# Performance work log

Measured on AMD Instinct MI355X. Metric: run time of the kernel, lower is better.

## Reference

```python
import jax, jax.numpy as jnp
import numpy as np

FACTOR = 8
IN_DIM = 4096
OUT_DIM = 4096


def setup_inputs() -> dict:
    key = jax.random.key(0)
    kx, ka, ks = jax.random.split(key, 3)
    x = jax.random.normal(kx, (4, 2048, IN_DIM), dtype=jnp.float32)
    a = jax.random.normal(ka, (FACTOR, FACTOR, FACTOR), dtype=jnp.float32) * 0.1
    s = jax.random.normal(ks, (FACTOR, OUT_DIM // FACTOR, IN_DIM // FACTOR), dtype=jnp.float32) * 0.05
    return {"x": x, "a": a, "s": s}


def reference(x, a, s):
    f = a.shape[0]
    out_dim = a.shape[1] * s.shape[1]
    in_dim = a.shape[2] * s.shape[2]
    # Batched Kronecker product: (f, a_rows*k, a_cols*p) then sum over batch dim f.
    # weight[a*k + ?, c*p + ?] = sum_b a[b, ar, ac] * s[b, kr, pc]
    p = jnp.einsum('bac,bkp->bakcp', a, s)  # (f, f, out/f, f, in/f)
    weight = p.reshape(f, out_dim, in_dim).sum(axis=0)  # (out, in)
    return x @ weight.T
```

## Files before the change

### kernel.cpp

```cpp
#include <hip/hip_runtime.h>
#include <hip/hip_bf16.h>
#include <stdint.h>

namespace {

constexpr int MTOT = 8192;
constexpr int NTOT = 4096;
constexpr int KTOT = 4096;

constexpr int BM = 256, BN = 256, BK = 32;
constexpr int NT = KTOT / BK;

typedef __attribute__((ext_vector_type(8))) short bf16x8;
typedef __attribute__((ext_vector_type(4))) float f32x4;

__device__ inline unsigned short to_bf16(float f) {
    union { float f; uint32_t u; } v; v.f = f;
    return (unsigned short)((v.u + 0x7FFFu + ((v.u >> 16) & 1u)) >> 16);
}

__global__ __launch_bounds__(256) void convert_x_kernel(const float* __restrict__ x,
                                                        unsigned short* __restrict__ xb) {
    int idx = blockIdx.x * 256 + threadIdx.x;
    const f32x4* xv = reinterpret_cast<const f32x4*>(x);
    f32x4 v0 = xv[2 * idx];
    f32x4 v1 = xv[2 * idx + 1];
    union { bf16x8 v; unsigned short s[8]; } o;
    o.s[0] = to_bf16(v0.x); o.s[1] = to_bf16(v0.y);
    o.s[2] = to_bf16(v0.z); o.s[3] = to_bf16(v0.w);
    o.s[4] = to_bf16(v1.x); o.s[5] = to_bf16(v1.y);
    o.s[6] = to_bf16(v1.z); o.s[7] = to_bf16(v1.w);
    reinterpret_cast<bf16x8*>(xb)[idx] = o.v;
}

__global__ __launch_bounds__(256) void gen_w_kernel(const float* __restrict__ a,
                                                    const float* __restrict__ s,
                                                    unsigned short* __restrict__ w) {
    int idx = blockIdx.x * 256 + threadIdx.x;
    int o  = idx >> 9;
    int i8 = idx & 511;
    int i0 = i8 * 8;
    int obig = o >> 9, orow = o & 511;
    int ibig = i0 >> 9, icol = i0 & 511;

    float acc[8];
#pragma unroll
    for (int j = 0; j < 8; ++j) acc[j] = 0.f;

#pragma unroll
    for (int b = 0; b < 8; ++b) {
        float av = a[b * 64 + obig * 8 + ibig];
        const f32x4* sv = reinterpret_cast<const f32x4*>(s + b * 512 * 512 + orow * 512 + icol);
        f32x4 s0 = sv[0], s1 = sv[1];
        acc[0] += av * s0.x; acc[1] += av * s0.y; acc[2] += av * s0.z; acc[3] += av * s0.w;
        acc[4] += av * s1.x; acc[5] += av * s1.y; acc[6] += av * s1.z; acc[7] += av * s1.w;
    }
    union { bf16x8 v; unsigned short q[8]; } ov;
#pragma unroll
    for (int j = 0; j < 8; ++j) ov.q[j] = to_bf16(acc[j]);
    reinterpret_cast<bf16x8*>(w)[idx] = ov.v;
}

__global__ __launch_bounds__(512, 2)
void gemm_bt_kernel(const unsigned short* __restrict__ A,
                    const unsigned short* __restrict__ B,
                    float* __restrict__ C) {
    __shared__ __align__(16) unsigned short As[4][BM][BK];
    __shared__ __align__(16) unsigned short Bs[4][BN][BK];

    int bid = blockIdx.x;
    int swz = (bid & 7) * 64 + (bid >> 3);
    int bm = swz >> 4;
    int bn = swz & 15;

    int tid  = threadIdx.x;
    int wid  = tid >> 6;
    int lane = tid & 63;
    int wm = wid >> 2, wn = wid & 3;

    int srow  = lane >> 2;
    int sslot = (lane & 3) ^ ((srow >> 1) & 3);
    const unsigned short* ag0 = A + (size_t)(bm * BM + wid * 16 + srow) * KTOT + sslot * 8;
    const unsigned short* ag1 = ag0 + (size_t)128 * KTOT;
    const unsigned short* bg0 = B + (size_t)(bn * BN + wid * 16 + srow) * KTOT + sslot * 8;
    const unsigned short* bg1 = bg0 + (size_t)128 * KTOT;

    int rl    = lane & 15;
    int rslot = (lane >> 4) ^ ((rl >> 1) & 3);

    f32x4 acc[8][4];
#pragma unroll
    for (int m = 0; m < 8; ++m)
#pragma unroll
        for (int n = 0; n < 4; ++n) acc[m][n] = (f32x4)0.f;

    auto STAGE_A = [&](int s, int k0) {
        __builtin_amdgcn_global_load_lds(
            (const __attribute__((address_space(1))) void*)(ag0 + k0),
            (__attribute__((address_space(3))) void*)&As[s][wid * 16][0], 16, 0, 0);
        __builtin_amdgcn_global_load_lds(
            (const __attribute__((address_space(1))) void*)(ag1 + k0),
            (__attribute__((address_space(3))) void*)&As[s][128 + wid * 16][0], 16, 0, 0);
    };
    auto STAGE_B = [&](int s, int k0) {
        __builtin_amdgcn_global_load_lds(
            (const __attribute__((address_space(1))) void*)(bg0 + k0),
            (__attribute__((address_space(3))) void*)&Bs[s][wid * 16][0], 16, 0, 0);
        __builtin_amdgcn_global_load_lds(
            (const __attribute__((address_space(1))) void*)(bg1 + k0),
            (__attribute__((address_space(3))) void*)&Bs[s][128 + wid * 16][0], 16, 0, 0);
    };

    auto LDA = [&](int s, int mi) -> bf16x8 {
        return *reinterpret_cast<const bf16x8*>(&As[s][wm * 128 + mi * 16 + rl][rslot * 8]);
    };
    auto LDB = [&](int s, int ni) -> bf16x8 {
        return *reinterpret_cast<const bf16x8*>(&Bs[s][wn * 64 + ni * 16 + rl][rslot * 8]);
    };

    bf16x8 fa[4], fb[4], ga[4], pa[4], pb[4];

    STAGE_A(0, 0);          STAGE_B(0, 0);
    STAGE_A(1, BK);         STAGE_B(1, BK);
    STAGE_A(2, 2 * BK);     STAGE_B(2, 2 * BK);
    asm volatile("s_waitcnt vmcnt(4)" ::: "memory");
    __builtin_amdgcn_s_barrier();
#pragma unroll
    for (int m = 0; m < 4; ++m) fa[m] = LDA(0, m);
#pragma unroll
    for (int n = 0; n < 4; ++n) fb[n] = LDB(0, n);

    for (int tb = 0; tb < NT; tb += 4) {
#pragma unroll
        for (int u = 0; u < 4; ++u) {
            const int t  = tb + u;
            const int s  = u;
            const int nx = (u + 1) & 3;
            const int ss = (u + 3) & 3;
            const bool st = (t + 3) < NT;
            const int k0 = (t + 3) * BK;

#pragma unroll
            for (int m = 0; m < 4; ++m) ga[m] = LDA(s, m + 4);
            if (st) STAGE_A(ss, k0);
            asm volatile("s_waitcnt lgkmcnt(4)" ::: "memory");
            __builtin_amdgcn_sched_barrier(0);
            __builtin_amdgcn_s_setprio(1);
#pragma unroll
            for (int m = 0; m < 4; ++m)
#pragma unroll
                for (int n = 0; n < 4; ++n)
                    acc[m][n] = __builtin_amdgcn_mfma_f32_16x16x32_bf16(fa[m], fb[n], acc[m][n], 0, 0, 0);
            __builtin_amdgcn_s_setprio(0);

#pragma unroll
            for (int m = 0; m < 4; ++m) pa[m] = LDA(nx, m);
#pragma unroll
            for (int n = 0; n < 4; ++n) pb[n] = LDB(nx, n);
            if (st) STAGE_B(ss, k0);
            asm volatile("s_waitcnt lgkmcnt(8)" ::: "memory");
            __builtin_amdgcn_sched_barrier(0);
            __builtin_amdgcn_s_setprio(1);
#pragma unroll
            for (int m = 0; m < 4; ++m)
#pragma unroll
                for (int n = 0; n < 4; ++n)
                    acc[m + 4][n] = __builtin_amdgcn_mfma_f32_16x16x32_bf16(ga[m], fb[n], acc[m + 4][n], 0, 0, 0);
            __builtin_amdgcn_s_setprio(0);

            asm volatile("s_waitcnt vmcnt(4)" ::: "memory");
            __builtin_amdgcn_s_barrier();

#pragma unroll
            for (int m = 0; m < 4; ++m) fa[m] = pa[m];
#pragma unroll
            for (int n = 0; n < 4; ++n) fb[n] = pb[n];
        }
    }

    int crow0 = bm * BM + wm * 128 + (lane >> 4) * 4;
    int ccol0 = bn * BN + wn * 64 + (lane & 15);
#pragma unroll
    for (int m = 0; m < 8; ++m)
#pragma unroll
        for (int n = 0; n < 4; ++n)
#pragma unroll
            for (int j = 0; j < 4; ++j) {
                size_t r = (size_t)(crow0 + m * 16 + j);
                size_t c = (size_t)(ccol0 + n * 16);
                C[r * NTOT + c] = acc[m][n][j];
            }
}

}

extern "C" void kernel_launch(void* const* d_in, const int* in_sizes, int n_in,
                              void* d_out, int out_size, void* d_ws, size_t ws_size,
                              hipStream_t stream) {
    const float* x = (const float*)d_in[0];
    const float* a = (const float*)d_in[1];
    const float* s = (const float*)d_in[2];
    float* out = (float*)d_out;

    unsigned short* xb = (unsigned short*)d_ws;
    unsigned short* wb = xb + (size_t)MTOT * KTOT;

    convert_x_kernel<<<(MTOT * KTOT / 8) / 256, 256, 0, stream>>>(x, xb);
    gen_w_kernel<<<(NTOT * KTOT / 8) / 256, 256, 0, stream>>>(a, s, wb);
    gemm_bt_kernel<<<(MTOT / 256) * (NTOT / 256), 512, 0, stream>>>(xb, wb, out);
}
```

Before: 293.9 us.

## Use 4 waves per block with 128x128 warp tiles in bf16 GEMM

Shrinks the GEMM block from 8 waves to 4. Each wave now computes a 128x128 output tile with 64 accumulators instead of 128x64, and staging is rebalanced so each wave loads 4 row groups. The register prefetch of next-stage fragments across iterations is removed: each iteration loads all of its A/B fragments from LDS and then issues two MFMA halves. This cuts LDS read traffic per FLOP, but it raises register pressure, halves waves per CU, and removes the LDS-to-register overlap.

```diff
diff --git a/kernel.cpp b/kernel.cpp
--- a/kernel.cpp
+++ b/kernel.cpp
@@ -61,7 +61,7 @@
     reinterpret_cast<bf16x8*>(w)[idx] = ov.v;
 }
 
-__global__ __launch_bounds__(512, 2)
+__global__ __launch_bounds__(256, 1)
 void gemm_bt_kernel(const unsigned short* __restrict__ A,
                     const unsigned short* __restrict__ B,
                     float* __restrict__ C) {
@@ -76,114 +76,101 @@
     int tid  = threadIdx.x;
     int wid  = tid >> 6;
     int lane = tid & 63;
-    int wm = wid >> 2, wn = wid & 3;
+    int wm = wid >> 1, wn = wid & 1;
 
     int srow  = lane >> 2;
     int sslot = (lane & 3) ^ ((srow >> 1) & 3);
-    const unsigned short* ag0 = A + (size_t)(bm * BM + wid * 16 + srow) * KTOT + sslot * 8;
-    const unsigned short* ag1 = ag0 + (size_t)128 * KTOT;
-    const unsigned short* bg0 = B + (size_t)(bn * BN + wid * 16 + srow) * KTOT + sslot * 8;
-    const unsigned short* bg1 = bg0 + (size_t)128 * KTOT;
+    const unsigned short* ag = A + (size_t)(bm * BM + wid * 64 + srow) * KTOT + sslot * 8;
+    const unsigned short* bg = B + (size_t)(bn * BN + wid * 64 + srow) * KTOT + sslot * 8;
 
     int rl    = lane & 15;
     int rslot = (lane >> 4) ^ ((rl >> 1) & 3);
 
-    f32x4 acc[8][4];
+    f32x4 acc[8][8];
 #pragma unroll
     for (int m = 0; m < 8; ++m)
 #pragma unroll
-        for (int n = 0; n < 4; ++n) acc[m][n] = (f32x4)0.f;
+        for (int n = 0; n < 8; ++n) acc[m][n] = (f32x4)0.f;
 
     auto STAGE_A = [&](int s, int k0) {
-        __builtin_amdgcn_global_load_lds(
-            (const __attribute__((address_space(1))) void*)(ag0 + k0),
-            (__attribute__((address_space(3))) void*)&As[s][wid * 16][0], 16, 0, 0);
-        __builtin_amdgcn_global_load_lds(
-            (const __attribute__((address_space(1))) void*)(ag1 + k0),
-            (__attribute__((address_space(3))) void*)&As[s][128 + wid * 16][0], 16, 0, 0);
+#pragma unroll
+        for (int g = 0; g < 4; ++g)
+            __builtin_amdgcn_global_load_lds(
+                (const __attribute__((address_space(1))) void*)(ag + (size_t)g * 16 * KTOT + k0),
+                (__attribute__((address_space(3))) void*)&As[s][wid * 64 + g * 16][0], 16, 0, 0);
     };
     auto STAGE_B = [&](int s, int k0) {
-        __builtin_amdgcn_global_load_lds(
-            (const __attribute__((address_space(1))) void*)(bg0 + k0),
-            (__attribute__((address_space(3))) void*)&Bs[s][wid * 16][0], 16, 0, 0);
-        __builtin_amdgcn_global_load_lds(
-            (const __attribute__((address_space(1))) void*)(bg1 + k0),
-            (__attribute__((address_space(3))) void*)&Bs[s][128 + wid * 16][0], 16, 0, 0);
+#pragma unroll
+        for (int g = 0; g < 4; ++g)
+            __builtin_amdgcn_global_load_lds(
+                (const __attribute__((address_space(1))) void*)(bg + (size_t)g * 16 * KTOT + k0),
+                (__attribute__((address_space(3))) void*)&Bs[s][wid * 64 + g * 16][0], 16, 0, 0);
     };
 
     auto LDA = [&](int s, int mi) -> bf16x8 {
         return *reinterpret_cast<const bf16x8*>(&As[s][wm * 128 + mi * 16 + rl][rslot * 8]);
     };
     auto LDB = [&](int s, int ni) -> bf16x8 {
-        return *reinterpret_cast<const bf16x8*>(&Bs[s][wn * 64 + ni * 16 + rl][rslot * 8]);
+        return *reinterpret_cast<const bf16x8*>(&Bs[s][wn * 128 + ni * 16 + rl][rslot * 8]);
     };
-
-    bf16x8 fa[4], fb[4], ga[4], pa[4], pb[4];
 
     STAGE_A(0, 0);          STAGE_B(0, 0);
     STAGE_A(1, BK);         STAGE_B(1, BK);
     STAGE_A(2, 2 * BK);     STAGE_B(2, 2 * BK);
-    asm volatile("s_waitcnt vmcnt(4)" ::: "memory");
+    asm volatile("s_waitcnt vmcnt(16)" ::: "memory");
     __builtin_amdgcn_s_barrier();
-#pragma unroll
-    for (int m = 0; m < 4; ++m) fa[m] = LDA(0, m);
-#pragma unroll
-    for (int n = 0; n < 4; ++n) fb[n] = LDB(0, n);
 
     for (int tb = 0; tb < NT; tb += 4) {
 #pragma unroll
         for (int u = 0; u < 4; ++u) {
             const int t  = tb + u;
             const int s  = u;
-            const int nx = (u + 1) & 3;
             const int ss = (u + 3) & 3;
             const bool st = (t + 3) < NT;
             const int k0 = (t + 3) * BK;
 
+            bf16x8 fa[8], fb[8];
+            if (st) STAGE_A(ss, k0);
 #pragma unroll
-            for (int m = 0; m < 4; ++m) ga[m] = LDA(s, m + 4);
-            if (st) STAGE_A(ss, k0);
+            for (int m = 0; m < 8; ++m) fa[m] = LDA(s, m);
+#pragma unroll
+            for (int n = 0; n < 4; ++n) fb[n] = LDB(s, n);
+            if (st) STAGE_B(ss, k0);
+#pragma unroll
+            for (int n = 4; n < 8; ++n) fb[n] = LDB(s, n);
+
             asm volatile("s_waitcnt lgkmcnt(4)" ::: "memory");
             __builtin_amdgcn_sched_barrier(0);
             __builtin_amdgcn_s_setprio(1);
 #pragma unroll
-            for (int m = 0; m < 4; ++m)
+            for (int m = 0; m < 8; ++m)
 #pragma unroll
                 for (int n = 0; n < 4; ++n)
                     acc[m][n] = __builtin_amdgcn_mfma_f32_16x16x32_bf16(fa[m], fb[n], acc[m][n], 0, 0, 0);
             __builtin_amdgcn_s_setprio(0);
 
-#pragma unroll
-            for (int m = 0; m < 4; ++m) pa[m] = LDA(nx, m);
-#pragma unroll
-            for (int n = 0; n < 4; ++n) pb[n] = LDB(nx, n);
-            if (st) STAGE_B(ss, k0);
-            asm volatile("s_waitcnt lgkmcnt(8)" ::: "memory");
+            asm volatile("s_waitcnt lgkmcnt(0)" ::: "memory");
             __builtin_amdgcn_sched_barrier(0);
             __builtin_amdgcn_s_setprio(1);
 #pragma unroll
-            for (int m = 0; m < 4; ++m)
+            for (int m = 0; m < 8; ++m)
 #pragma unroll
-                for (int n = 0; n < 4; ++n)
-                    acc[m + 4][n] = __builtin_amdgcn_mfma_f32_16x16x32_bf16(ga[m], fb[n], acc[m + 4][n], 0, 0, 0);
+                for (int n = 4; n < 8; ++n)
+                    acc[m][n] = __builtin_amdgcn_mfma_f32_16x16x32_bf16(fa[m], fb[n], acc[m][n], 0, 0, 0);
             __builtin_amdgcn_s_setprio(0);
 
-            asm volatile("s_waitcnt vmcnt(4)" ::: "memory");
+            if (st) { asm volatile("s_waitcnt vmcnt(8)" ::: "memory"); }
+            else    { asm volatile("s_waitcnt vmcnt(0)" ::: "memory"); }
             __builtin_amdgcn_s_barrier();
-
-#pragma unroll
-            for (int m = 0; m < 4; ++m) fa[m] = pa[m];
-#pragma unroll
-            for (int n = 0; n < 4; ++n) fb[n] = pb[n];
         }
     }
 
     int crow0 = bm * BM + wm * 128 + (lane >> 4) * 4;
-    int ccol0 = bn * BN + wn * 64 + (lane & 15);
+    int ccol0 = bn * BN + wn * 128 + (lane & 15);
 #pragma unroll
     for (int m = 0; m < 8; ++m)
 #pragma unroll
-        for (int n = 0; n < 4; ++n)
+        for (int n = 0; n < 8; ++n)
 #pragma unroll
             for (int j = 0; j < 4; ++j) {
                 size_t r = (size_t)(crow0 + m * 16 + j);
@@ -207,5 +194,5 @@
 
     convert_x_kernel<<<(MTOT * KTOT / 8) / 256, 256, 0, stream>>>(x, xb);
     gen_w_kernel<<<(NTOT * KTOT / 8) / 256, 256, 0, stream>>>(a, s, wb);
-    gemm_bt_kernel<<<(MTOT / 256) * (NTOT / 256), 512, 0, stream>>>(xb, wb, out);
+    gemm_bt_kernel<<<(MTOT / BM) * (NTOT / BN), 256, 0, stream>>>(xb, wb, out);
 }
```

After: 393.3 us. 33.8% more time.
